# Kernel optimization log

Hardware: AMD Instinct MI355X
Metric: run time of the kernel (lower is better)

The kernel has to match this reference:

```python
import jax, jax.numpy as jnp
import numpy as np

B, C_IN, H, W_SP = 16, 128, 56, 56
C_OUT, KH, KW = 256, 3, 3
STRIDE = (1, 1)
PADDING = (1, 1)


def setup_inputs() -> dict:
    key = jax.random.key(0)
    kx, kw = jax.random.split(key)
    x = jax.random.normal(kx, (B, C_IN, H, W_SP), dtype=jnp.float32)
    W = jax.random.normal(kw, (C_OUT, C_IN, KH, KW), dtype=jnp.float32) * 0.01
    b = jnp.zeros((C_OUT,), dtype=jnp.float32)
    return {"x": x, "W": W, "b": b}


def reference(x, W, b):
    # NCHW direct convolution, same math as the nested-loop torch module.
    out = jax.lax.conv_general_dilated(
        x, W,
        window_strides=STRIDE,
        padding=[(PADDING[0], PADDING[0]), (PADDING[1], PADDING[1])],
        dimension_numbers=("NCHW", "OIHW", "NCHW"),
    )
    return out + b[None, :, None, None]
```

## Files before the change

### kernel.cpp

```cpp
#include <hip/hip_runtime.h>

typedef __attribute__((ext_vector_type(8))) short short8;
typedef __attribute__((ext_vector_type(4))) float f32x4;

#define CI    128
#define CO_   256
#define HW_   56
#define PLANE 3136
#define NB    16
#define STOT  50176
#define KTOT  1152
#define OUTN  802816

#define XT_BYTES   12845056ull
#define WP_USHORTS 294912
#define WS_NEED    (12845056ull + 589824ull + 256ull)

__device__ __forceinline__ unsigned short f2bf(float f) {
  unsigned u = __float_as_uint(f);
  u += 0x7FFFu + ((u >> 16) & 1u);
  return (unsigned short)(u >> 16);
}

__device__ __forceinline__ void gload16(void* lds, const void* g) {
  __builtin_amdgcn_global_load_lds(
      (const __attribute__((address_space(1))) unsigned int*)g,
      (__attribute__((address_space(3))) unsigned int*)lds, 16, 0, 0);
}

__global__ __launch_bounds__(256) void prep_fused(const float* __restrict__ X,
                                                  const float* __restrict__ W,
                                                  unsigned short* __restrict__ Xt,
                                                  unsigned short* __restrict__ Wp) {
  const int t = threadIdx.x;
  if (blockIdx.x < 1600) {
    __shared__ __align__(16) unsigned short tile[32][132];
    const int bx = blockIdx.x;
    const int n   = bx / 100;
    const int rem = bx % 100;
    const int cib = rem / 25;
    const int spb = rem % 25;
    const int sp0 = spb * 128;
    const float* src = X + (size_t)(n * CI + cib * 32) * PLANE;
#pragma unroll
    for (int j = 0; j < 4; ++j) {
      int f = t + 256 * j;
      int ci  = f >> 5;
      int sp4 = (f & 31) * 4;
      if (sp0 + sp4 < PLANE) {
        f32x4 v = *(const f32x4*)(src + (size_t)ci * PLANE + sp0 + sp4);
#pragma unroll
        for (int e = 0; e < 4; ++e) tile[ci][sp4 + e] = f2bf(v[e]);
      }
    }
    __syncthreads();
    unsigned short* dst = Xt + ((size_t)n * PLANE + sp0) * CI + cib * 32;
#pragma unroll
    for (int j = 0; j < 2; ++j) {
      int g = t + 256 * j;
      int sp = g >> 2;
      int q  = g & 3;
      if (sp0 + sp < PLANE) {
        short8 v;
#pragma unroll
        for (int e = 0; e < 8; ++e) v[e] = (short)tile[q * 8 + e][sp];
        *(short8*)(dst + (size_t)sp * CI + q * 8) = v;
      }
    }
  } else {
    const int c = (blockIdx.x - 1600) * 256 + t;
    const int kt   = c >> 11;
    const int i3   = (c >> 9) & 3;
    const int tt   = c & 511;
    const int ks   = i3 >> 1;
    const int half = i3 & 1;
    const int row  = half * 128 + (tt >> 2);
    const int swzq = (tt & 3) ^ ((tt >> 3) & 3);
    const int r    = kt >> 1;
    const int cib  = kt & 1;
    const int ci0  = cib * 64 + ks * 32 + swzq * 8;
    short8 v;
#pragma unroll
    for (int e = 0; e < 8; ++e)
      v[e] = (short)f2bf(W[(size_t)row * KTOT + (size_t)(ci0 + e) * 9 + r]);
    *(short8*)(Wp + (size_t)c * 8) = v;
    if (c < 16) {
      short8 z = {0, 0, 0, 0, 0, 0, 0, 0};
      *(short8*)(Wp + WP_USHORTS + c * 8) = z;
    }
  }
}

#define MFMA_Q(MH, NH)                                                                 \
  __builtin_amdgcn_s_setprio(1);                                                       \
  _Pragma("unroll") for (int ks = 0; ks < 2; ++ks)                                     \
  _Pragma("unroll") for (int m = 0; m < 4; ++m)                                        \
  _Pragma("unroll") for (int n = 0; n < 2; ++n)                                        \
    acc[(MH)*4 + m][(NH)*2 + n] = __builtin_amdgcn_mfma_f32_16x16x32_bf16(             \
        aF[m][ks], bF[(NH)*2 + n][ks], acc[(MH)*4 + m][(NH)*2 + n], 0, 0, 0);          \
  __builtin_amdgcn_s_setprio(0);

__global__ __launch_bounds__(512, 2) void conv_gemm(const unsigned short* __restrict__ Xt,
                                                    const unsigned short* __restrict__ Wp,
                                                    const float* __restrict__ bias,
                                                    float* __restrict__ out) {
  __shared__ __align__(1024) char smem[131072];
  const int t    = threadIdx.x;
  const int lane = t & 63;
  const int wid  = t >> 6;
  const int wm   = wid >> 2, wn = wid & 3;

  const int orig = blockIdx.x;
  const int xcd = orig & 7, idx = orig >> 3;
  const int spt = (xcd < 4 ? xcd * 25 : 100 + (xcd - 4) * 24) + idx;

  const int kgB = (t & 3) ^ ((t >> 3) & 3);
  const int S0 = spt * 256 + (t >> 2);
  const int S1 = S0 + 128;
  const int hw0 = S0 % PLANE, h0 = hw0 / HW_, w0 = hw0 - h0 * HW_;
  const int hw1 = S1 % PLANE, h1 = hw1 / HW_, w1 = hw1 - h1 * HW_;
  int vm0 = 0, vm1 = 0;
#pragma unroll
  for (int r = 0; r < 9; ++r) {
    int dh = r / 3 - 1, dw = r % 3 - 1;
    vm0 |= (int)(((unsigned)(h0 + dh) < HW_) & ((unsigned)(w0 + dw) < HW_)) << r;
    vm1 |= (int)(((unsigned)(h1 + dh) < HW_) & ((unsigned)(w1 + dw) < HW_)) << r;
  }
  const char* xb0 = (const char*)Xt + ((size_t)S0 * CI + kgB * 8) * 2;
  const char* xb1 = (const char*)Xt + ((size_t)S1 * CI + kgB * 8) * 2;
  const char* zb  = (const char*)(Wp + WP_USHORTS) + (t & 3) * 16;
  const char* wpA = (const char*)Wp + t * 16;

  const int swz  = ((lane >> 4) ^ ((lane >> 1) & 3)) * 16;
  const int aoff = (wm * 128 + (lane & 15)) * 64 + swz;
  const int boff = 32768 + (wn * 64 + (lane & 15)) * 64 + swz;

  f32x4 acc[8][4];
  const f32x4 zf = {0.f, 0.f, 0.f, 0.f};
#pragma unroll
  for (int m = 0; m < 8; ++m)
#pragma unroll
    for (int n = 0; n < 4; ++n) acc[m][n] = zf;

  auto SA = [&](int kt1, int i, char* buf) {
    gload16(buf + (i >> 1) * 16384 + (i & 1) * 8192 + wid * 1024,
            wpA + (size_t)(kt1 * 4 + i) * 8192);
  };
  auto SB = [&](int kt1, int i, char* buf) {
    const int ks = i >> 1, half = i & 1;
    const int r = kt1 >> 1, cib = kt1 & 1;
    const int dh = r / 3 - 1, dw = r % 3 - 1;
    const int ro = dh * HW_ + dw;
    const bool v = ((half ? vm1 : vm0) >> r) & 1;
    const char* src = (half ? xb1 : xb0) + ro * 256 + cib * 128 + ks * 64;
    gload16(buf + 32768 + ks * 16384 + half * 8192 + wid * 1024, v ? src : zb);
  };

  {
    char* b0 = smem;
#pragma unroll
    for (int i = 0; i < 4; ++i) { SA(0, i, b0); SB(0, i, b0); }
  }
  __syncthreads();

#pragma unroll
  for (int kt = 0; kt < 18; ++kt) {
    char* cur = smem + (kt & 1) * 65536;
    char* nxt = smem + ((kt + 1) & 1) * 65536;
    const char* ca = cur + aoff;
    const char* cb = cur + boff;
    short8 aF[4][2], bF[4][2];

#pragma unroll
    for (int m = 0; m < 4; ++m) {
      aF[m][0] = *(const short8*)(ca + m * 1024);
      aF[m][1] = *(const short8*)(ca + 16384 + m * 1024);
    }
#pragma unroll
    for (int n = 0; n < 2; ++n) {
      bF[n][0] = *(const short8*)(cb + n * 1024);
      bF[n][1] = *(const short8*)(cb + 16384 + n * 1024);
    }
    if (kt < 17) { SA(kt + 1, 0, nxt); SA(kt + 1, 1, nxt); SB(kt + 1, 0, nxt); }
    __builtin_amdgcn_s_barrier();
    MFMA_Q(0, 0)
    __builtin_amdgcn_s_barrier();

#pragma unroll
    for (int n = 0; n < 2; ++n) {
      bF[2 + n][0] = *(const short8*)(cb + (2 + n) * 1024);
      bF[2 + n][1] = *(const short8*)(cb + 16384 + (2 + n) * 1024);
    }
    if (kt < 17) { SA(kt + 1, 2, nxt); SA(kt + 1, 3, nxt); SB(kt + 1, 1, nxt); }
    __builtin_amdgcn_s_barrier();
    MFMA_Q(0, 1)
    __builtin_amdgcn_s_barrier();

#pragma unroll
    for (int m = 0; m < 4; ++m) {
      aF[m][0] = *(const short8*)(ca + 4096 + m * 1024);
      aF[m][1] = *(const short8*)(ca + 16384 + 4096 + m * 1024);
    }
    if (kt < 17) { SB(kt + 1, 2, nxt); SB(kt + 1, 3, nxt); }
    __builtin_amdgcn_s_barrier();
    MFMA_Q(1, 1)
    __builtin_amdgcn_s_barrier();

    MFMA_Q(1, 0)

    __syncthreads();
  }

#pragma unroll
  for (int nf = 0; nf < 4; ++nf) {
    int S = spt * 256 + wn * 64 + nf * 16 + (lane & 15);
    int nimg = S / PLANE, hw = S - nimg * PLANE;
    float* ob = out + (size_t)nimg * OUTN + hw;
#pragma unroll
    for (int mf = 0; mf < 8; ++mf) {
      int cob = wm * 128 + mf * 16 + (lane >> 4) * 4;
#pragma unroll
      for (int r2 = 0; r2 < 4; ++r2)
        ob[(size_t)(cob + r2) * PLANE] = acc[mf][nf][r2] + bias[cob + r2];
    }
  }
}

__global__ __launch_bounds__(256) void conv_naive(const float* __restrict__ X,
                                                  const float* __restrict__ W,
                                                  const float* __restrict__ bias,
                                                  float* __restrict__ out) {
  int idx = blockIdx.x * 256 + threadIdx.x;
  int hw = idx % PLANE;
  int co = (idx / PLANE) & 255;
  int n  = idx / (PLANE * 256);
  int h = hw / HW_, w = hw - h * HW_;
  float acc = bias[co];
  const float* xp = X + (size_t)n * CI * PLANE;
  const float* wp = W + (size_t)co * KTOT;
  for (int ci = 0; ci < CI; ++ci) {
#pragma unroll
    for (int kh = 0; kh < 3; ++kh) {
      int y = h + kh - 1;
      if ((unsigned)y >= HW_) continue;
#pragma unroll
      for (int kw = 0; kw < 3; ++kw) {
        int x = w + kw - 1;
        if ((unsigned)x >= HW_) continue;
        acc += xp[(size_t)ci * PLANE + y * HW_ + x] * wp[ci * 9 + kh * 3 + kw];
      }
    }
  }
  out[idx] = acc;
}

extern "C" void kernel_launch(void* const* d_in, const int* in_sizes, int n_in,
                              void* d_out, int out_size, void* d_ws, size_t ws_size,
                              hipStream_t stream) {
  (void)in_sizes; (void)n_in; (void)out_size;
  const float* X = (const float*)d_in[0];
  const float* W = (const float*)d_in[1];
  const float* b = (const float*)d_in[2];
  float* out = (float*)d_out;
  if (ws_size >= WS_NEED) {
    unsigned short* Xt = (unsigned short*)d_ws;
    unsigned short* Wp = (unsigned short*)((char*)d_ws + XT_BYTES);
    prep_fused<<<1744, 256, 0, stream>>>(X, W, Xt, Wp);
    conv_gemm<<<196, 512, 0, stream>>>(Xt, Wp, b, out);
  } else {
    conv_naive<<<(NB * CO_ * PLANE + 255) / 256, 256, 0, stream>>>(X, W, b, out);
  }
}
```

Baseline: 50.96 us.

## Replace double-buffered K loop with 4-stage LDS ring and vmcnt waits

```diff
diff --git a/kernel.cpp b/kernel.cpp
--- a/kernel.cpp
+++ b/kernel.cpp
@@ -26,6 +26,10 @@
   __builtin_amdgcn_global_load_lds(
       (const __attribute__((address_space(1))) unsigned int*)g,
       (__attribute__((address_space(3))) unsigned int*)lds, 16, 0, 0);
+}
+
+template <int N> __device__ __forceinline__ void vmwait() {
+  asm volatile("s_waitcnt vmcnt(%0)" ::"n"(N) : "memory");
 }
 
 __global__ __launch_bounds__(256) void prep_fused(const float* __restrict__ X,
@@ -68,37 +72,28 @@
       }
     }
   } else {
-    const int c = (blockIdx.x - 1600) * 256 + t;
-    const int kt   = c >> 11;
-    const int i3   = (c >> 9) & 3;
-    const int tt   = c & 511;
-    const int ks   = i3 >> 1;
-    const int half = i3 & 1;
-    const int row  = half * 128 + (tt >> 2);
-    const int swzq = (tt & 3) ^ ((tt >> 3) & 3);
-    const int r    = kt >> 1;
-    const int cib  = kt & 1;
-    const int ci0  = cib * 64 + ks * 32 + swzq * 8;
+    const int u = (blockIdx.x - 1600) * 256 + t;
+    const int rcbmt = u >> 9;
+    const int p     = u & 511;
+    const int mt  = rcbmt & 1;
+    const int rcb = rcbmt >> 1;
+    const int cb  = rcb & 3;
+    const int r   = rcb >> 2;
+    const int col = p >> 2;
+    const int kg  = (p & 3) ^ ((col >> 1) & 3);
+    const int co  = mt * 128 + col;
+    const int ci0 = cb * 32 + kg * 8;
     short8 v;
 #pragma unroll
     for (int e = 0; e < 8; ++e)
-      v[e] = (short)f2bf(W[(size_t)row * KTOT + (size_t)(ci0 + e) * 9 + r]);
-    *(short8*)(Wp + (size_t)c * 8) = v;
-    if (c < 16) {
+      v[e] = (short)f2bf(W[(size_t)co * KTOT + (size_t)(ci0 + e) * 9 + r]);
+    *(short8*)(Wp + (size_t)u * 8) = v;
+    if (u < 16) {
       short8 z = {0, 0, 0, 0, 0, 0, 0, 0};
-      *(short8*)(Wp + WP_USHORTS + c * 8) = z;
-    }
-  }
-}
-
-#define MFMA_Q(MH, NH)                                                                 \
-  __builtin_amdgcn_s_setprio(1);                                                       \
-  _Pragma("unroll") for (int ks = 0; ks < 2; ++ks)                                     \
-  _Pragma("unroll") for (int m = 0; m < 4; ++m)                                        \
-  _Pragma("unroll") for (int n = 0; n < 2; ++n)                                        \
-    acc[(MH)*4 + m][(NH)*2 + n] = __builtin_amdgcn_mfma_f32_16x16x32_bf16(             \
-        aF[m][ks], bF[(NH)*2 + n][ks], acc[(MH)*4 + m][(NH)*2 + n], 0, 0, 0);          \
-  __builtin_amdgcn_s_setprio(0);
+      *(short8*)(Wp + WP_USHORTS + u * 8) = z;
+    }
+  }
+}
 
 __global__ __launch_bounds__(512, 2) void conv_gemm(const unsigned short* __restrict__ Xt,
                                                     const unsigned short* __restrict__ Wp,
@@ -133,7 +128,7 @@
 
   const int swz  = ((lane >> 4) ^ ((lane >> 1) & 3)) * 16;
   const int aoff = (wm * 128 + (lane & 15)) * 64 + swz;
-  const int boff = 32768 + (wn * 64 + (lane & 15)) * 64 + swz;
+  const int boff = 16384 + (wn * 64 + (lane & 15)) * 64 + swz;
 
   f32x4 acc[8][4];
   const f32x4 zf = {0.f, 0.f, 0.f, 0.f};
@@ -142,73 +137,47 @@
 #pragma unroll
     for (int n = 0; n < 4; ++n) acc[m][n] = zf;
 
-  auto SA = [&](int kt1, int i, char* buf) {
-    gload16(buf + (i >> 1) * 16384 + (i & 1) * 8192 + wid * 1024,
-            wpA + (size_t)(kt1 * 4 + i) * 8192);
+  auto SA = [&](int s1, int j, char* buf) {
+    gload16(buf + j * 8192 + wid * 1024, wpA + (size_t)s1 * 16384 + j * 8192);
   };
-  auto SB = [&](int kt1, int i, char* buf) {
-    const int ks = i >> 1, half = i & 1;
-    const int r = kt1 >> 1, cib = kt1 & 1;
+  auto SB = [&](int s1, int j, char* buf) {
+    const int r = s1 >> 2, cb = s1 & 3;
     const int dh = r / 3 - 1, dw = r % 3 - 1;
     const int ro = dh * HW_ + dw;
-    const bool v = ((half ? vm1 : vm0) >> r) & 1;
-    const char* src = (half ? xb1 : xb0) + ro * 256 + cib * 128 + ks * 64;
-    gload16(buf + 32768 + ks * 16384 + half * 8192 + wid * 1024, v ? src : zb);
+    const bool v = ((j ? vm1 : vm0) >> r) & 1;
+    const char* src = (j ? xb1 : xb0) + ro * 256 + cb * 64;
+    gload16(buf + 16384 + j * 8192 + wid * 1024, v ? src : zb);
   };
-
-  {
-    char* b0 = smem;
-#pragma unroll
-    for (int i = 0; i < 4; ++i) { SA(0, i, b0); SB(0, i, b0); }
-  }
-  __syncthreads();
-
-#pragma unroll
-  for (int kt = 0; kt < 18; ++kt) {
-    char* cur = smem + (kt & 1) * 65536;
-    char* nxt = smem + ((kt + 1) & 1) * 65536;
-    const char* ca = cur + aoff;
-    const char* cb = cur + boff;
-    short8 aF[4][2], bF[4][2];
-
-#pragma unroll
-    for (int m = 0; m < 4; ++m) {
-      aF[m][0] = *(const short8*)(ca + m * 1024);
-      aF[m][1] = *(const short8*)(ca + 16384 + m * 1024);
-    }
-#pragma unroll
-    for (int n = 0; n < 2; ++n) {
-      bF[n][0] = *(const short8*)(cb + n * 1024);
-      bF[n][1] = *(const short8*)(cb + 16384 + n * 1024);
-    }
-    if (kt < 17) { SA(kt + 1, 0, nxt); SA(kt + 1, 1, nxt); SB(kt + 1, 0, nxt); }
+  auto STAGE = [&](int s1) {
+    char* nb = smem + (s1 & 3) * 32768;
+    SA(s1, 0, nb); SA(s1, 1, nb); SB(s1, 0, nb); SB(s1, 1, nb);
+  };
+
+  STAGE(0); STAGE(1); STAGE(2);
+
+#pragma unroll
+  for (int s = 0; s < 36; ++s) {
+    if (s <= 33)      vmwait<8>();
+    else if (s == 34) vmwait<4>();
+    else              vmwait<0>();
     __builtin_amdgcn_s_barrier();
-    MFMA_Q(0, 0)
-    __builtin_amdgcn_s_barrier();
-
-#pragma unroll
-    for (int n = 0; n < 2; ++n) {
-      bF[2 + n][0] = *(const short8*)(cb + (2 + n) * 1024);
-      bF[2 + n][1] = *(const short8*)(cb + 16384 + (2 + n) * 1024);
-    }
-    if (kt < 17) { SA(kt + 1, 2, nxt); SA(kt + 1, 3, nxt); SB(kt + 1, 1, nxt); }
-    __builtin_amdgcn_s_barrier();
-    MFMA_Q(0, 1)
-    __builtin_amdgcn_s_barrier();
-
-#pragma unroll
-    for (int m = 0; m < 4; ++m) {
-      aF[m][0] = *(const short8*)(ca + 4096 + m * 1024);
-      aF[m][1] = *(const short8*)(ca + 16384 + 4096 + m * 1024);
-    }
-    if (kt < 17) { SB(kt + 1, 2, nxt); SB(kt + 1, 3, nxt); }
-    __builtin_amdgcn_s_barrier();
-    MFMA_Q(1, 1)
-    __builtin_amdgcn_s_barrier();
-
-    MFMA_Q(1, 0)
-
-    __syncthreads();
+
+    if (s <= 32) STAGE(s + 3);
+
+    const char* rb = smem + (s & 3) * 32768;
+    short8 aF[8], bF[4];
+#pragma unroll
+    for (int m = 0; m < 8; ++m) aF[m] = *(const short8*)(rb + aoff + m * 1024);
+#pragma unroll
+    for (int n = 0; n < 4; ++n) bF[n] = *(const short8*)(rb + boff + n * 1024);
+
+    __builtin_amdgcn_s_setprio(1);
+#pragma unroll
+    for (int m = 0; m < 8; ++m)
+#pragma unroll
+      for (int n = 0; n < 4; ++n)
+        acc[m][n] = __builtin_amdgcn_mfma_f32_16x16x32_bf16(aF[m], bF[n], acc[m][n], 0, 0, 0);
+    __builtin_amdgcn_s_setprio(0);
   }
 
 #pragma unroll
```

After: 50.53 us. Within noise of the previous version (-0.8%).
